# Performance work log

Measured on AMD Instinct MI355X. Metric: run time of the kernel, lower is better.

## Reference

```python
import jax, jax.numpy as jnp
import numpy as np

N_LAYER = 4
N_HEAD = 12
D_MODEL = 768
SEQ_LEN = 2048
VOCAB = 50257
BATCH = 2


def _sinusoid_pe(seq_len, d_model):
    pos = np.arange(seq_len, dtype=np.float32)[:, None]
    div = np.exp(np.arange(0, d_model, 2, dtype=np.float32) * (-np.log(10000.0) / d_model))
    pe = np.zeros((seq_len, d_model), dtype=np.float32)
    pe[:, 0::2] = np.sin(pos * div)
    pe[:, 1::2] = np.cos(pos * div)
    return jnp.asarray(pe[None])  # [1, C, D]


def setup_inputs() -> dict:
    key = jax.random.key(0)
    ks = jax.random.split(key, 12)
    s = 0.02
    return {
        "features": jax.random.randint(ks[0], (BATCH, SEQ_LEN), 0, VOCAB),
        "targets": jax.random.randint(ks[1], (BATCH, SEQ_LEN), 0, VOCAB),
        "tok_embed": jax.random.normal(ks[2], (VOCAB, D_MODEL), jnp.float32) * s,
        "pos_emb": _sinusoid_pe(SEQ_LEN, D_MODEL),
        "ln1_w": jnp.ones((N_LAYER, D_MODEL), jnp.float32),
        "ln1_b": jnp.zeros((N_LAYER, D_MODEL), jnp.float32),
        "attn_w": jax.random.normal(ks[3], (N_LAYER, D_MODEL, 3 * D_MODEL), jnp.float32) * s,
        "attn_b": jnp.zeros((N_LAYER, 3 * D_MODEL), jnp.float32),
        "proj_w": jax.random.normal(ks[4], (N_LAYER, D_MODEL, D_MODEL), jnp.float32) * s,
        "proj_b": jnp.zeros((N_LAYER, D_MODEL), jnp.float32),
        "ln2_w": jnp.ones((N_LAYER, D_MODEL), jnp.float32),
        "ln2_b": jnp.zeros((N_LAYER, D_MODEL), jnp.float32),
        "ffn_w1": jax.random.normal(ks[5], (N_LAYER, D_MODEL, 4 * D_MODEL), jnp.float32) * s,
        "ffn_b1": jnp.zeros((N_LAYER, 4 * D_MODEL), jnp.float32),
        "ffn_w2": jax.random.normal(ks[6], (N_LAYER, 4 * D_MODEL, D_MODEL), jnp.float32) * s,
        "ffn_b2": jnp.zeros((N_LAYER, D_MODEL), jnp.float32),
        "lnf_w": jnp.ones((D_MODEL,), jnp.float32),
        "lnf_b": jnp.zeros((D_MODEL,), jnp.float32),
        "final_w": jax.random.normal(ks[7], (D_MODEL, VOCAB), jnp.float32) * s,
    }


def _layernorm(x, w, b, eps=1e-5):
    mu = jnp.mean(x, axis=-1, keepdims=True)
    var = jnp.var(x, axis=-1, keepdims=True)
    return (x - mu) * jax.lax.rsqrt(var + eps) * w + b


def _attention(x, wqkv, bqkv, wo, bo):
    B, C, E = x.shape
    dh = E // N_HEAD
    qkv = x @ wqkv + bqkv  # [B, C, 3E]
    q, k, v = jnp.split(qkv, 3, axis=-1)
    q = q.reshape(B, C, N_HEAD, dh)
    k = k.reshape(B, C, N_HEAD, dh)
    v = v.reshape(B, C, N_HEAD, dh)
    att = jnp.einsum("bqhd,bkhd->bhqk", q, k) / jnp.sqrt(jnp.float32(dh))
    causal = jnp.tril(jnp.ones((C, C), bool))
    att = jnp.where(causal, att, -jnp.inf)
    att = jax.nn.softmax(att, axis=-1)
    y = jnp.einsum("bhqk,bkhd->bqhd", att, v).reshape(B, C, E)
    return y @ wo + bo


def reference(features, targets, tok_embed, pos_emb, ln1_w, ln1_b, attn_w, attn_b,
              proj_w, proj_b, ln2_w, ln2_b, ffn_w1, ffn_b1, ffn_w2, ffn_b2,
              lnf_w, lnf_b, final_w):
    C = features.shape[1]
    x = tok_embed[features] + pos_emb[:, :C]
    for l in range(N_LAYER):
        h = _layernorm(x, ln1_w[l], ln1_b[l])
        x = x + _attention(h, attn_w[l], attn_b[l], proj_w[l], proj_b[l])
        h = _layernorm(x, ln2_w[l], ln2_b[l])
        h = jax.nn.gelu(h @ ffn_w1[l] + ffn_b1[l], approximate=False) @ ffn_w2[l] + ffn_b2[l]
        x = x + h
    x = _layernorm(x, lnf_w, lnf_b)
    logits = x @ final_w  # [B, C, V]
    logp = jax.nn.log_softmax(logits, axis=-1)
    tgt = targets.reshape(-1)
    valid = tgt != -1
    tgt_safe = jnp.where(valid, tgt, 0)
    nll = -jnp.take_along_axis(logp.reshape(-1, logits.shape[-1]), tgt_safe[:, None], axis=1)[:, 0]
    loss = jnp.sum(jnp.where(valid, nll, 0.0)) / jnp.maximum(jnp.sum(valid), 1)
    return logits, loss
```

## Files before the change

kernel.cpp:

```cpp
#include <hip/hip_runtime.h>
#include <math.h>

#define N_LAYER 4
#define N_HEAD  12
#define D_MODEL 768
#define SEQ     2048
#define VOCAB   50257
#define BATCH   2
#define MROWS   (BATCH*SEQ)

typedef __bf16 bf16;
typedef __bf16 bf16x8 __attribute__((ext_vector_type(8)));
typedef float  f32x4  __attribute__((ext_vector_type(4)));
typedef short  short8v __attribute__((ext_vector_type(8)));

__device__ __forceinline__ void gload16(const bf16* g, const bf16* l) {
    __builtin_amdgcn_global_load_lds(
        (const __attribute__((address_space(1))) void*)g,
        (__attribute__((address_space(3))) void*)l,
        16, 0, 0);
}

__global__ __launch_bounds__(256) void embed_kernel(
    const int* __restrict__ feat, const float* __restrict__ tok,
    const float* __restrict__ pos, float* __restrict__ x)
{
    int row = blockIdx.x;
    int cpos = row & (SEQ - 1);
    int tid = feat[row];
    const float* te = tok + (size_t)tid * D_MODEL;
    const float* pe = pos + (size_t)cpos * D_MODEL;
    float* xr = x + (size_t)row * D_MODEL;
    for (int c = threadIdx.x; c < D_MODEL; c += 256)
        xr[c] = te[c] + pe[c];
}

__global__ __launch_bounds__(256) void ln_kernel(
    const float* __restrict__ x, const float* __restrict__ w,
    const float* __restrict__ b, bf16* __restrict__ out)
{
    int row = blockIdx.x;
    const float* xr = x + (size_t)row * D_MODEL;
    float lv[3];
    float s = 0.f, ss = 0.f;
#pragma unroll
    for (int i = 0; i < 3; i++) {
        float v = xr[threadIdx.x + i * 256];
        lv[i] = v; s += v; ss += v * v;
    }
#pragma unroll
    for (int o = 32; o; o >>= 1) { s += __shfl_down(s, o, 64); ss += __shfl_down(ss, o, 64); }
    __shared__ float red[8];
    int wid = threadIdx.x >> 6;
    if ((threadIdx.x & 63) == 0) { red[wid] = s; red[wid + 4] = ss; }
    __syncthreads();
    s  = red[0] + red[1] + red[2] + red[3];
    ss = red[4] + red[5] + red[6] + red[7];
    float mu  = s * (1.f / D_MODEL);
    float var = ss * (1.f / D_MODEL) - mu * mu;
    float rs  = rsqrtf(var + 1e-5f);
#pragma unroll
    for (int i = 0; i < 3; i++) {
        int c = threadIdx.x + i * 256;
        out[(size_t)row * D_MODEL + c] = (bf16)((lv[i] - mu) * rs * w[c] + b[c]);
    }
}

__global__ __launch_bounds__(256) void transpose_conv_kernel(
    const float* __restrict__ W, bf16* __restrict__ Wt, int K, int N)
{
    int l = blockIdx.z;
    const float* Wl = W + (size_t)l * K * N;
    bf16* Wtl = Wt + (size_t)l * K * N;
    __shared__ float tile[32][33];
    int k0 = blockIdx.y * 32, n0 = blockIdx.x * 32;
    for (int idx = threadIdx.x; idx < 1024; idx += 256) {
        int i = idx >> 5, j = idx & 31;
        int n = n0 + j;
        tile[i][j] = (n < N) ? Wl[(size_t)(k0 + i) * N + n] : 0.f;
    }
    __syncthreads();
    for (int idx = threadIdx.x; idx < 1024; idx += 256) {
        int j = idx >> 5, i = idx & 31;
        int n = n0 + j;
        if (n < N) Wtl[(size_t)n * K + k0 + i] = (bf16)tile[i][j];
    }
}

__global__ __launch_bounds__(256) void vtrans_kernel(
    const bf16* __restrict__ qkv, bf16* __restrict__ vT)
{
    int j0 = blockIdx.x * 64, h = blockIdx.y, b = blockIdx.z;
    __shared__ bf16 t[64][72];
    const bf16* src = qkv + ((size_t)b * SEQ + j0) * (3 * D_MODEL) + 2 * D_MODEL + h * 64;
    int tid = threadIdx.x;
#pragma unroll
    for (int i = 0; i < 2; i++) {
        int c = tid + i * 256;
        int j = c >> 3, d8 = (c & 7) * 8;
        *(short8v*)&t[j][d8] = *(const short8v*)&src[(size_t)j * (3 * D_MODEL) + d8];
    }
    __syncthreads();
    bf16* dst = vT + ((size_t)(b * N_HEAD + h) * 64) * SEQ;
#pragma unroll
    for (int i = 0; i < 2; i++) {
        int c = tid + i * 256;
        int d = c >> 3, j8 = (c & 7) * 8;
        bf16 tmp[8];
#pragma unroll
        for (int e = 0; e < 8; e++) tmp[e] = t[j8 + e][d];
        *(short8v*)&dst[(size_t)d * SEQ + j0 + j8] = *(const short8v*)tmp;
    }
}

template<bool BIAS, bool GELU_, int OUTM, bool SWZ, bool LSE, int SPLITK>
__global__ __launch_bounds__(256) void gemm_kernel(
    const bf16* __restrict__ A, const bf16* __restrict__ Bt,
    const float* __restrict__ bias, void* __restrict__ Cout,
    float* __restrict__ rowsum,
    int M, int N, int K)
{
    __shared__ __align__(16) bf16 As[128 * 32];
    __shared__ __align__(16) bf16 Bs[128 * 32];
    int tid = threadIdx.x;
    int lane = tid & 63, wid = tid >> 6;

    int Kslice = K / SPLITK;
    int kbase = (SPLITK > 1) ? (int)blockIdx.z * Kslice : 0;

    int nbx = gridDim.x;
    int bid = blockIdx.y * nbx + blockIdx.x;
    if (SWZ) {
        int nwg = nbx * gridDim.y;
        int q = nwg >> 3, r = nwg & 7;
        int xcd = bid & 7, loc = bid >> 3;
        bid = (xcd < r ? xcd * (q + 1) : r * (q + 1) + (xcd - r) * q) + loc;
    }
    int row0 = (bid % nbx) * 128;
    int col0 = (bid / nbx) * 128;

    int wr = (wid >> 1) * 64, wc = (wid & 1) * 64;

    int srow = wid * 16 + (lane >> 2);
    int selem = (lane & 3) * 8;
    const bf16* Ab0 = A + (size_t)(row0 + srow) * K + kbase + selem;
    const bf16* Ab1 = Ab0 + (size_t)64 * K;
    int bn0 = col0 + srow;      if (bn0 >= N) bn0 = N - 1;
    int bn1 = col0 + srow + 64; if (bn1 >= N) bn1 = N - 1;
    const bf16* Bb0 = Bt + (size_t)bn0 * K + kbase + selem;
    const bf16* Bb1 = Bt + (size_t)bn1 * K + kbase + selem;
    bf16* ldsA0 = As + wid * 512;
    bf16* ldsA1 = As + (wid + 4) * 512;
    bf16* ldsB0 = Bs + wid * 512;
    bf16* ldsB1 = Bs + (wid + 4) * 512;

    f32x4 acc[4][4] = {};
    int fr = lane & 15, fg8 = (lane >> 4) * 8;

    for (int k0 = 0; k0 < Kslice; k0 += 32) {
        if (k0) __syncthreads();
        gload16(Ab0 + k0, ldsA0);
        gload16(Ab1 + k0, ldsA1);
        gload16(Bb0 + k0, ldsB0);
        gload16(Bb1 + k0, ldsB1);
        __syncthreads();

        bf16x8 af[4], bfr[4];
#pragma unroll
        for (int m = 0; m < 4; m++) af[m] = *(const bf16x8*)&As[(wr + m * 16 + fr) * 32 + fg8];
#pragma unroll
        for (int n = 0; n < 4; n++) bfr[n] = *(const bf16x8*)&Bs[(wc + n * 16 + fr) * 32 + fg8];
#pragma unroll
        for (int m = 0; m < 4; m++)
#pragma unroll
            for (int n = 0; n < 4; n++)
                acc[m][n] = __builtin_amdgcn_mfma_f32_16x16x32_bf16(af[m], bfr[n], acc[m][n], 0, 0, 0);
    }

    int g = lane >> 4;
    bool addbias = BIAS && (SPLITK == 1 || blockIdx.z == 0);
    float lsum[4][4];
#pragma unroll
    for (int m = 0; m < 4; m++)
#pragma unroll
        for (int r = 0; r < 4; r++) lsum[m][r] = 0.f;

#pragma unroll
    for (int m = 0; m < 4; m++) {
#pragma unroll
        for (int n = 0; n < 4; n++) {
            int col = col0 + wc + n * 16 + fr;
            bool ok = (col < N);
            float bv = (addbias && ok) ? bias[col] : 0.f;
#pragma unroll
            for (int r = 0; r < 4; r++) {
                int row = row0 + wr + m * 16 + g * 4 + r;
                float v = acc[m][n][r] + bv;
                if (GELU_) v = 0.5f * v * (1.f + erff(v * 0.70710678118f));
                if (ok) {
                    if (OUTM == 0)
                        __builtin_nontemporal_store(v, &((float*)Cout)[(size_t)row * N + col]);
                    else if (OUTM == 1)
                        ((bf16*)Cout)[(size_t)row * N + col] = (bf16)v;
                    else if (SPLITK > 1)
                        atomicAdd(&((float*)Cout)[(size_t)row * N + col], v);
                    else
                        ((float*)Cout)[(size_t)row * N + col] += v;
                }
                if (LSE) lsum[m][r] += ok ? __expf(v) : 0.f;
            }
        }
    }

    if (LSE) {
#pragma unroll
        for (int m = 0; m < 4; m++)
#pragma unroll
            for (int r = 0; r < 4; r++) {
                float s = lsum[m][r];
#pragma unroll
                for (int o = 1; o < 16; o <<= 1) s += __shfl_xor(s, o, 64);
                lsum[m][r] = s;
            }
        if (fr == 0) {
#pragma unroll
            for (int m = 0; m < 4; m++)
#pragma unroll
                for (int r = 0; r < 4; r++)
                    atomicAdd(&rowsum[row0 + wr + m * 16 + g * 4 + r], lsum[m][r]);
        }
    }
}

__global__ __launch_bounds__(256) void attn_kernel(
    const bf16* __restrict__ qkv, const bf16* __restrict__ vT, bf16* __restrict__ y)
{
    int qt = blockIdx.x, h = blockIdx.y, b = blockIdx.z;
    const size_t rs = 3 * D_MODEL;
    int tid = threadIdx.x, lane = tid & 63, wid = tid >> 6;
    int fr = lane & 15, g = lane >> 4;
    int wq = qt * 64 + wid * 16;

    const bf16* qb = qkv + (size_t)b * SEQ * rs + h * 64;
    const bf16* kb = qb + D_MODEL;
    const bf16* vb = vT + ((size_t)(b * N_HEAD + h) * 64) * SEQ;

    __shared__ bf16 Ps[4][16][72];

    bf16x8 aq[2];
#pragma unroll
    for (int kk = 0; kk < 2; kk++)
        aq[kk] = *(const bf16x8*)&qb[(size_t)(wq + fr) * rs + kk * 32 + g * 8];

    f32x4 acco[4] = {};
    float mrow[4], lrow[4];
#pragma unroll
    for (int r = 0; r < 4; r++) { mrow[r] = -1e30f; lrow[r] = 0.f; }

    int jmax = qt * 64;
    for (int j0 = 0; j0 <= jmax; j0 += 64) {
        f32x4 accs[4] = {};
#pragma unroll
        for (int n = 0; n < 4; n++)
#pragma unroll
            for (int kk = 0; kk < 2; kk++) {
                bf16x8 bk = *(const bf16x8*)&kb[(size_t)(j0 + n * 16 + fr) * rs + kk * 32 + g * 8];
                accs[n] = __builtin_amdgcn_mfma_f32_16x16x32_bf16(aq[kk], bk, accs[n], 0, 0, 0);
            }

        bool diag = (j0 == jmax);
#pragma unroll
        for (int n = 0; n < 4; n++) {
            int jc = j0 + n * 16 + fr;
#pragma unroll
            for (int r = 0; r < 4; r++) {
                float sv = accs[n][r] * 0.125f;
                if (diag) { int irow = wq + g * 4 + r; if (jc > irow) sv = -1e30f; }
                accs[n][r] = sv;
            }
        }

        float pscale[4];
#pragma unroll
        for (int r = 0; r < 4; r++) {
            float pm = fmaxf(fmaxf(accs[0][r], accs[1][r]), fmaxf(accs[2][r], accs[3][r]));
#pragma unroll
            for (int o = 1; o < 16; o <<= 1) pm = fmaxf(pm, __shfl_xor(pm, o, 64));
            float mnew = fmaxf(mrow[r], pm);
            float corr = __expf(mrow[r] - mnew);
            mrow[r] = mnew;
            float ls = 0.f;
#pragma unroll
            for (int n = 0; n < 4; n++) {
                float p = __expf(accs[n][r] - mnew);
                accs[n][r] = p; ls += p;
            }
#pragma unroll
            for (int o = 1; o < 16; o <<= 1) ls += __shfl_xor(ls, o, 64);
            lrow[r] = lrow[r] * corr + ls;
            pscale[r] = corr;
        }
#pragma unroll
        for (int n = 0; n < 4; n++)
#pragma unroll
            for (int r = 0; r < 4; r++) acco[n][r] *= pscale[r];

#pragma unroll
        for (int n = 0; n < 4; n++)
#pragma unroll
            for (int r = 0; r < 4; r++)
                Ps[wid][g * 4 + r][n * 16 + fr] = (bf16)accs[n][r];

        bf16x8 ap[2];
#pragma unroll
        for (int kk = 0; kk < 2; kk++)
            ap[kk] = *(const bf16x8*)&Ps[wid][fr][kk * 32 + g * 8];
#pragma unroll
        for (int kk = 0; kk < 2; kk++)
#pragma unroll
            for (int n = 0; n < 4; n++) {
                bf16x8 bv = *(const bf16x8*)&vb[(size_t)(n * 16 + fr) * SEQ + j0 + kk * 32 + g * 8];
                acco[n] = __builtin_amdgcn_mfma_f32_16x16x32_bf16(ap[kk], bv, acco[n], 0, 0, 0);
            }
    }

    bf16* yb = y + (size_t)b * SEQ * D_MODEL + h * 64;
#pragma unroll
    for (int n = 0; n < 4; n++)
#pragma unroll
        for (int r = 0; r < 4; r++) {
            int row = wq + g * 4 + r;
            yb[(size_t)row * D_MODEL + n * 16 + fr] = (bf16)(acco[n][r] / lrow[r]);
        }
}

__global__ __launch_bounds__(256) void loss_nll_kernel(
    const float* __restrict__ logits, const float* __restrict__ rowsum,
    const int* __restrict__ tgt, float* __restrict__ accum)
{
    int row = blockIdx.x * 256 + threadIdx.x;
    if (row >= MROWS) return;
    int t = tgt[row];
    if (t >= 0) {
        float nll = logf(rowsum[row]) - logits[(size_t)row * VOCAB + t];
        atomicAdd(accum, nll);
        atomicAdd(accum + 1, 1.f);
    }
}

__global__ void loss_final_kernel(const float* __restrict__ accum, float* __restrict__ out)
{
    out[0] = accum[0] / fmaxf(accum[1], 1.f);
}

extern "C" void kernel_launch(void* const* d_in, const int* in_sizes, int n_in,
                              void* d_out, int out_size, void* d_ws, size_t ws_size,
                              hipStream_t stream)
{
    const int*   feat  = (const int*)d_in[0];
    const int*   tgt   = (const int*)d_in[1];
    const float* tok   = (const float*)d_in[2];
    const float* pos   = (const float*)d_in[3];
    const float* ln1w  = (const float*)d_in[4];
    const float* ln1b  = (const float*)d_in[5];
    const float* attnw = (const float*)d_in[6];
    const float* attnb = (const float*)d_in[7];
    const float* projw = (const float*)d_in[8];
    const float* projb = (const float*)d_in[9];
    const float* ln2w  = (const float*)d_in[10];
    const float* ln2b  = (const float*)d_in[11];
    const float* fw1   = (const float*)d_in[12];
    const float* fb1   = (const float*)d_in[13];
    const float* fw2   = (const float*)d_in[14];
    const float* fb2   = (const float*)d_in[15];
    const float* lnfw  = (const float*)d_in[16];
    const float* lnfb  = (const float*)d_in[17];
    const float* finw  = (const float*)d_in[18];

    char* ws = (char*)d_ws;
    size_t off = 0;
    auto alloc = [&](size_t bytes) -> void* {
        void* p = ws + off; off += (bytes + 255) & ~(size_t)255; return p;
    };
    float* x     = (float*)alloc((size_t)MROWS * D_MODEL * 4);
    bf16*  h     = (bf16*) alloc((size_t)MROWS * D_MODEL * 2);
    bf16*  big   = (bf16*) alloc((size_t)MROWS * 4 * D_MODEL * 2);
    bf16*  ybuf  = (bf16*) alloc((size_t)MROWS * D_MODEL * 2);
    bf16*  vT    = (bf16*) alloc((size_t)BATCH * N_HEAD * 64 * SEQ * 2);
    bf16*  awt   = (bf16*) alloc((size_t)N_LAYER * 3 * D_MODEL * D_MODEL * 2);
    bf16*  pwt   = (bf16*) alloc((size_t)N_LAYER * D_MODEL * D_MODEL * 2);
    bf16*  f1wt  = (bf16*) alloc((size_t)N_LAYER * 4 * D_MODEL * D_MODEL * 2);
    bf16*  f2wt  = (bf16*) alloc((size_t)N_LAYER * 4 * D_MODEL * D_MODEL * 2);
    bf16*  fwt   = (bf16*) alloc((size_t)VOCAB * D_MODEL * 2);
    float* rowsum= (float*)alloc((size_t)MROWS * 4);
    float* accum = (float*)alloc(256);

    float* logits = (float*)d_out;
    float* lossp  = (float*)d_out + (size_t)MROWS * VOCAB;

    dim3 blk(256);
    transpose_conv_kernel<<<dim3(3 * D_MODEL / 32, D_MODEL / 32, N_LAYER), blk, 0, stream>>>(attnw, awt, D_MODEL, 3 * D_MODEL);
    transpose_conv_kernel<<<dim3(D_MODEL / 32, D_MODEL / 32, N_LAYER), blk, 0, stream>>>(projw, pwt, D_MODEL, D_MODEL);
    transpose_conv_kernel<<<dim3(4 * D_MODEL / 32, D_MODEL / 32, N_LAYER), blk, 0, stream>>>(fw1, f1wt, D_MODEL, 4 * D_MODEL);
    transpose_conv_kernel<<<dim3(D_MODEL / 32, 4 * D_MODEL / 32, N_LAYER), blk, 0, stream>>>(fw2, f2wt, 4 * D_MODEL, D_MODEL);
    transpose_conv_kernel<<<dim3((VOCAB + 31) / 32, D_MODEL / 32, 1), blk, 0, stream>>>(finw, fwt, D_MODEL, VOCAB);

    embed_kernel<<<MROWS, blk, 0, stream>>>(feat, tok, pos, x);

    for (int l = 0; l < N_LAYER; l++) {
        ln_kernel<<<MROWS, blk, 0, stream>>>(x, ln1w + l * D_MODEL, ln1b + l * D_MODEL, h);
        gemm_kernel<true, false, 1, false, false, 1><<<dim3(MROWS / 128, (3 * D_MODEL) / 128), blk, 0, stream>>>(
            h, awt + (size_t)l * 3 * D_MODEL * D_MODEL, attnb + l * 3 * D_MODEL, big, nullptr,
            MROWS, 3 * D_MODEL, D_MODEL);
        vtrans_kernel<<<dim3(SEQ / 64, N_HEAD, BATCH), blk, 0, stream>>>(big, vT);
        attn_kernel<<<dim3(SEQ / 64, N_HEAD, BATCH), blk, 0, stream>>>(big, vT, ybuf);
        gemm_kernel<true, false, 2, false, false, 2><<<dim3(MROWS / 128, D_MODEL / 128, 2), blk, 0, stream>>>(
            ybuf, pwt + (size_t)l * D_MODEL * D_MODEL, projb + l * D_MODEL, x, nullptr,
            MROWS, D_MODEL, D_MODEL);
        ln_kernel<<<MROWS, blk, 0, stream>>>(x, ln2w + l * D_MODEL, ln2b + l * D_MODEL, h);
        gemm_kernel<true, true, 1, false, false, 1><<<dim3(MROWS / 128, (4 * D_MODEL) / 128), blk, 0, stream>>>(
            h, f1wt + (size_t)l * 4 * D_MODEL * D_MODEL, fb1 + l * 4 * D_MODEL, big, nullptr,
            MROWS, 4 * D_MODEL, D_MODEL);
        gemm_kernel<true, false, 2, false, false, 2><<<dim3(MROWS / 128, D_MODEL / 128, 2), blk, 0, stream>>>(
            big, f2wt + (size_t)l * 4 * D_MODEL * D_MODEL, fb2 + l * D_MODEL, x, nullptr,
            MROWS, D_MODEL, 4 * D_MODEL);
    }

    ln_kernel<<<MROWS, blk, 0, stream>>>(x, lnfw, lnfb, h);

    hipMemsetAsync(rowsum, 0, (size_t)MROWS * 4, stream);
    hipMemsetAsync(accum, 0, 8, stream);

    gemm_kernel<false, false, 0, true, true, 1><<<dim3(MROWS / 128, (VOCAB + 127) / 128), blk, 0, stream>>>(
        h, fwt, nullptr, logits, rowsum, MROWS, VOCAB, D_MODEL);

    loss_nll_kernel<<<(MROWS + 255) / 256, blk, 0, stream>>>(logits, rowsum, tgt, accum);
    loss_final_kernel<<<1, 1, 0, stream>>>(accum, lossp);

    (void)in_sizes; (void)n_in; (void)out_size; (void)ws_size;
}
```

Before: 2.440 ms.

## Use persistent vocab-panel kernel for logits GEMM with in-block row-tile loop

The logits GEMM moves into a dedicated kernel. Each block owns one 128-column vocab panel and half of the rows, and loops over 16 row tiles, so each panel of B rows is reused across tiles from cache. It replaces the XCD swizzle and the nontemporal stores with plain stores. The grid shrinks to about 786 blocks, each doing serial work, which cuts parallelism and may hurt latency hiding. The exp-sum accumulation for the loss stays fused in the epilogue.

```diff
diff --git a/kernel.cpp b/kernel.cpp
--- a/kernel.cpp
+++ b/kernel.cpp
@@ -113,11 +113,10 @@
     }
 }
 
-template<bool BIAS, bool GELU_, int OUTM, bool SWZ, bool LSE, int SPLITK>
+template<bool BIAS, bool GELU_, int OUTM, int SPLITK>
 __global__ __launch_bounds__(256) void gemm_kernel(
     const bf16* __restrict__ A, const bf16* __restrict__ Bt,
     const float* __restrict__ bias, void* __restrict__ Cout,
-    float* __restrict__ rowsum,
     int M, int N, int K)
 {
     __shared__ __align__(16) bf16 As[128 * 32];
@@ -128,16 +127,8 @@
     int Kslice = K / SPLITK;
     int kbase = (SPLITK > 1) ? (int)blockIdx.z * Kslice : 0;
 
-    int nbx = gridDim.x;
-    int bid = blockIdx.y * nbx + blockIdx.x;
-    if (SWZ) {
-        int nwg = nbx * gridDim.y;
-        int q = nwg >> 3, r = nwg & 7;
-        int xcd = bid & 7, loc = bid >> 3;
-        bid = (xcd < r ? xcd * (q + 1) : r * (q + 1) + (xcd - r) * q) + loc;
-    }
-    int row0 = (bid % nbx) * 128;
-    int col0 = (bid / nbx) * 128;
+    int row0 = blockIdx.x * 128;
+    int col0 = blockIdx.y * 128;
 
     int wr = (wid >> 1) * 64, wc = (wid & 1) * 64;
 
@@ -179,11 +170,6 @@
 
     int g = lane >> 4;
     bool addbias = BIAS && (SPLITK == 1 || blockIdx.z == 0);
-    float lsum[4][4];
-#pragma unroll
-    for (int m = 0; m < 4; m++)
-#pragma unroll
-        for (int r = 0; r < 4; r++) lsum[m][r] = 0.f;
 
 #pragma unroll
     for (int m = 0; m < 4; m++) {
@@ -199,7 +185,7 @@
                 if (GELU_) v = 0.5f * v * (1.f + erff(v * 0.70710678118f));
                 if (ok) {
                     if (OUTM == 0)
-                        __builtin_nontemporal_store(v, &((float*)Cout)[(size_t)row * N + col]);
+                        ((float*)Cout)[(size_t)row * N + col] = v;
                     else if (OUTM == 1)
                         ((bf16*)Cout)[(size_t)row * N + col] = (bf16)v;
                     else if (SPLITK > 1)
@@ -207,12 +193,85 @@
                     else
                         ((float*)Cout)[(size_t)row * N + col] += v;
                 }
-                if (LSE) lsum[m][r] += ok ? __expf(v) : 0.f;
-            }
-        }
-    }
-
-    if (LSE) {
+            }
+        }
+    }
+}
+
+__global__ __launch_bounds__(256) void gemm_logits_kernel(
+    const bf16* __restrict__ A, const bf16* __restrict__ Bt,
+    float* __restrict__ Cout, float* __restrict__ rowsum,
+    int N, int K)
+{
+    __shared__ __align__(16) bf16 As[128 * 32];
+    __shared__ __align__(16) bf16 Bs[128 * 32];
+    int tid = threadIdx.x, lane = tid & 63, wid = tid >> 6;
+    int panel = blockIdx.x >> 1, half = blockIdx.x & 1;
+    int col0 = panel * 128;
+    int wr = (wid >> 1) * 64, wc = (wid & 1) * 64;
+    int fr = lane & 15, fg8 = (lane >> 4) * 8, g = lane >> 4;
+
+    int srow = wid * 16 + (lane >> 2);
+    int selem = (lane & 3) * 8;
+    int bn0 = col0 + srow;      if (bn0 >= N) bn0 = N - 1;
+    int bn1 = col0 + srow + 64; if (bn1 >= N) bn1 = N - 1;
+    const bf16* Bb0 = Bt + (size_t)bn0 * K + selem;
+    const bf16* Bb1 = Bt + (size_t)bn1 * K + selem;
+    bf16* ldsA0 = As + wid * 512;
+    bf16* ldsA1 = As + (wid + 4) * 512;
+    bf16* ldsB0 = Bs + wid * 512;
+    bf16* ldsB1 = Bs + (wid + 4) * 512;
+
+    for (int mt = 0; mt < 16; ++mt) {
+        int row0 = half * (MROWS / 2) + mt * 128;
+        const bf16* Ab0 = A + (size_t)(row0 + srow) * K + selem;
+        const bf16* Ab1 = Ab0 + (size_t)64 * K;
+
+        f32x4 acc[4][4] = {};
+        for (int k0 = 0; k0 < K; k0 += 32) {
+            __syncthreads();
+            gload16(Ab0 + k0, ldsA0);
+            gload16(Ab1 + k0, ldsA1);
+            gload16(Bb0 + k0, ldsB0);
+            gload16(Bb1 + k0, ldsB1);
+            __syncthreads();
+
+            bf16x8 af[4], bfr[4];
+#pragma unroll
+            for (int m = 0; m < 4; m++) af[m] = *(const bf16x8*)&As[(wr + m * 16 + fr) * 32 + fg8];
+#pragma unroll
+            for (int n = 0; n < 4; n++) bfr[n] = *(const bf16x8*)&Bs[(wc + n * 16 + fr) * 32 + fg8];
+#pragma unroll
+            for (int m = 0; m < 4; m++)
+#pragma unroll
+                for (int n = 0; n < 4; n++)
+                    acc[m][n] = __builtin_amdgcn_mfma_f32_16x16x32_bf16(af[m], bfr[n], acc[m][n], 0, 0, 0);
+        }
+
+        float lsum[4][4];
+#pragma unroll
+        for (int m = 0; m < 4; m++)
+#pragma unroll
+            for (int r = 0; r < 4; r++) lsum[m][r] = 0.f;
+
+#pragma unroll
+        for (int m = 0; m < 4; m++) {
+#pragma unroll
+            for (int n = 0; n < 4; n++) {
+                int col = col0 + wc + n * 16 + fr;
+                bool ok = (col < N);
+#pragma unroll
+                for (int r = 0; r < 4; r++) {
+                    int row = row0 + wr + m * 16 + g * 4 + r;
+                    float v = acc[m][n][r];
+                    if (ok) {
+                        Cout[(size_t)row * N + col] = v;
+                        lsum[m][r] += __expf(v);
+                    }
+                }
+            }
+        }
+
 #pragma unroll
         for (int m = 0; m < 4; m++)
 #pragma unroll
@@ -409,20 +468,20 @@
 
     for (int l = 0; l < N_LAYER; l++) {
         ln_kernel<<<MROWS, blk, 0, stream>>>(x, ln1w + l * D_MODEL, ln1b + l * D_MODEL, h);
-        gemm_kernel<true, false, 1, false, false, 1><<<dim3(MROWS / 128, (3 * D_MODEL) / 128), blk, 0, stream>>>(
-            h, awt + (size_t)l * 3 * D_MODEL * D_MODEL, attnb + l * 3 * D_MODEL, big, nullptr,
+        gemm_kernel<true, false, 1, 1><<<dim3(MROWS / 128, (3 * D_MODEL) / 128), blk, 0, stream>>>(
+            h, awt + (size_t)l * 3 * D_MODEL * D_MODEL, attnb + l * 3 * D_MODEL, big,
             MROWS, 3 * D_MODEL, D_MODEL);
         vtrans_kernel<<<dim3(SEQ / 64, N_HEAD, BATCH), blk, 0, stream>>>(big, vT);
         attn_kernel<<<dim3(SEQ / 64, N_HEAD, BATCH), blk, 0, stream>>>(big, vT, ybuf);
-        gemm_kernel<true, false, 2, false, false, 2><<<dim3(MROWS / 128, D_MODEL / 128, 2), blk, 0, stream>>>(
-            ybuf, pwt + (size_t)l * D_MODEL * D_MODEL, projb + l * D_MODEL, x, nullptr,
+        gemm_kernel<true, false, 2, 2><<<dim3(MROWS / 128, D_MODEL / 128, 2), blk, 0, stream>>>(
+            ybuf, pwt + (size_t)l * D_MODEL * D_MODEL, projb + l * D_MODEL, x,
             MROWS, D_MODEL, D_MODEL);
         ln_kernel<<<MROWS, blk, 0, stream>>>(x, ln2w + l * D_MODEL, ln2b + l * D_MODEL, h);
-        gemm_kernel<true, true, 1, false, false, 1><<<dim3(MROWS / 128, (4 * D_MODEL) / 128), blk, 0, stream>>>(
-            h, f1wt + (size_t)l * 4 * D_MODEL * D_MODEL, fb1 + l * 4 * D_MODEL, big, nullptr,
+        gemm_kernel<true, true, 1, 1><<<dim3(MROWS / 128, (4 * D_MODEL) / 128), blk, 0, stream>>>(
+            h, f1wt + (size_t)l * 4 * D_MODEL * D_MODEL, fb1 + l * 4 * D_MODEL, big,
             MROWS, 4 * D_MODEL, D_MODEL);
-        gemm_kernel<true, false, 2, false, false, 2><<<dim3(MROWS / 128, D_MODEL / 128, 2), blk, 0, stream>>>(
-            big, f2wt + (size_t)l * 4 * D_MODEL * D_MODEL, fb2 + l * D_MODEL, x, nullptr,
+        gemm_kernel<true, false, 2, 2><<<dim3(MROWS / 128, D_MODEL / 128, 2), blk, 0, stream>>>(
+            big, f2wt + (size_t)l * 4 * D_MODEL * D_MODEL, fb2 + l * D_MODEL, x,
             MROWS, D_MODEL, 4 * D_MODEL);
     }
 
@@ -431,8 +490,9 @@
     hipMemsetAsync(rowsum, 0, (size_t)MROWS * 4, stream);
     hipMemsetAsync(accum, 0, 8, stream);
 
-    gemm_kernel<false, false, 0, true, true, 1><<<dim3(MROWS / 128, (VOCAB + 127) / 128), blk, 0, stream>>>(
-        h, fwt, nullptr, logits, rowsum, MROWS, VOCAB, D_MODEL);
+    int npanel = (VOCAB + 127) / 128;
+    gemm_logits_kernel<<<dim3(npanel * 2), blk, 0, stream>>>(
+        h, fwt, logits, rowsum, VOCAB, D_MODEL);
 
     loss_nll_kernel<<<(MROWS + 255) / 256, blk, 0, stream>>>(logits, rowsum, tgt, accum);
     loss_final_kernel<<<1, 1, 0, stream>>>(accum, lossp);
```

Measured after the change: 2.571 ms. 1.05x slower.
